# Kernel tuning notes

Hardware: AMD Instinct MI355X
Metric: run time of the kernel (lower is better)

Reference implementation:

```python
import jax, jax.numpy as jnp
import numpy as np

B, S, D_IN, D_OUT, RANK = 4, 2048, 4096, 4096, 32
BLOCK = 16
Q_MAX = 7.0  # INT4: 2**(4-1) - 1


def quantize_uniform(x, block_size=BLOCK, q_max=Q_MAX):
    """Block-wise symmetric fake-quantize (round-to-nearest, clamp)."""
    orig_shape = x.shape
    xf = x.reshape(-1, block_size)
    amax = jnp.clip(jnp.max(jnp.abs(xf), axis=-1, keepdims=True), 1e-12, None)
    scale = amax / q_max
    xq = jnp.clip(jnp.round(xf / scale), -q_max, q_max) * scale
    return xq.reshape(orig_shape)


def setup_inputs() -> dict:
    key = jax.random.key(0)
    ks = jax.random.split(key, 7)
    x = jax.random.normal(ks[0], (B, S, D_IN), jnp.float32)
    smooth_scale = jax.random.uniform(ks[1], (D_IN,), jnp.float32, 0.5, 2.0)
    w_quantized = jax.random.normal(ks[2], (D_OUT, D_IN), jnp.float32) * 0.02
    lora_a = jax.random.normal(ks[3], (RANK, D_IN), jnp.float32) * 0.02
    lora_b = jax.random.normal(ks[4], (D_OUT, RANK), jnp.float32) * 0.02
    w_sparse = jax.random.normal(ks[5], (D_OUT, D_IN), jnp.float32) * 0.02
    bias = jax.random.normal(ks[6], (D_OUT,), jnp.float32) * 0.02
    return {"x": x, "smooth_scale": smooth_scale, "w_quantized": w_quantized,
            "lora_a": lora_a, "lora_b": lora_b, "w_sparse": w_sparse, "bias": bias}


def reference(x, smooth_scale, w_quantized, lora_a, lora_b, w_sparse, bias):
    # smoothing (SmoothQuant-style per-channel scale)
    x_smoothed = x * smooth_scale                      # [B,S,Din]
    # block-wise INT4 fake-quantize of the smoothed activations
    x_q = quantize_uniform(x_smoothed)                 # [B,S,Din]
    # quantized main path
    base_out = jnp.einsum('bsi,oi->bso', x_q, w_quantized)
    # low-rank SVD error-correction path
    svd_out = jnp.einsum('bsr,or->bso',
                         jnp.einsum('bsi,ri->bsr', x_smoothed, lora_a),
                         lora_b)
    # sparse-outlier path (unsmoothed x)
    sparse_out = jnp.einsum('bsi,oi->bso', x, w_sparse)
    return base_out + svd_out + sparse_out + bias
```

## Files before the change

kernel.cpp:

```cpp
#include <hip/hip_runtime.h>
#include <stdint.h>

typedef float  f32x4  __attribute__((ext_vector_type(4)));
typedef __bf16 bf16x8 __attribute__((ext_vector_type(8)));
typedef unsigned int   u32;
typedef unsigned short u16;
typedef unsigned long long u64;
typedef u32 u32x4 __attribute__((ext_vector_type(4)));

#define M_TOT 8192
#define N_TOT 4096
#define K_DIN 4096
#define RANK  32
#define KCAT  8320
#define NTILE 130

__device__ __forceinline__ u16 f2bf(float f) {
  union { float f; u32 u; } v; v.f = f;
  u32 r = v.u + 0x7fffu + ((v.u >> 16) & 1u);
  return (u16)(r >> 16);
}

__global__ void prep_as_k(const float* __restrict__ la, const float* __restrict__ ss,
                          u16* __restrict__ asb) {
  int i = blockIdx.x * 256 + threadIdx.x;
  f32x4 v = ((const f32x4*)la)[i];
  f32x4 s = ((const f32x4*)ss)[i & 1023];
  f32x4 p = v * s;
  alignas(8) u16 o[4] = { f2bf(p[0]), f2bf(p[1]), f2bf(p[2]), f2bf(p[3]) };
  *(u64*)(asb + 4 * (size_t)i) = *(const u64*)o;
}

__global__ void cvt_w_k(const float* __restrict__ in, u16* __restrict__ Bb, int colofs) {
  int i = blockIdx.x * 256 + threadIdx.x;
  f32x4 v = ((const f32x4*)in)[i];
  int r = i >> 10, c = (i & 1023) * 4;
  alignas(8) u16 o[4] = { f2bf(v[0]), f2bf(v[1]), f2bf(v[2]), f2bf(v[3]) };
  *(u64*)(Bb + (size_t)r * KCAT + colofs + c) = *(const u64*)o;
}

__global__ void cvt_lb_k(const float* __restrict__ in, u16* __restrict__ Bb) {
  int i = blockIdx.x * 256 + threadIdx.x;
  f32x4 v = ((const f32x4*)in)[i];
  int row = i >> 3, c = (i & 7) * 4;
  alignas(8) u16 o[4] = { f2bf(v[0]), f2bf(v[1]), f2bf(v[2]), f2bf(v[3]) };
  u16* rp = Bb + (size_t)row * KCAT;
  *(u64*)(rp + 2 * K_DIN + c) = *(const u64*)o;
  u16* zp = rp + 2 * K_DIN + RANK + (i & 7) * 12;
  *(u64*)(zp + 0) = 0; *(u64*)(zp + 4) = 0; *(u64*)(zp + 8) = 0;
}

__global__ void prep_x_k(const float* __restrict__ x, const float* __restrict__ ss,
                         u16* __restrict__ Ab) {
  int m = blockIdx.x;
  int t = threadIdx.x;
  const f32x4* xp = (const f32x4*)(x + (size_t)m * K_DIN + t * 16);
  const f32x4* sp = (const f32x4*)(ss + t * 16);
  float xs[16];
  alignas(16) u16 rb[16], qb[16];
  float amax = 0.0f;
  #pragma unroll
  for (int i = 0; i < 4; ++i) {
    f32x4 a = xp[i], s = sp[i];
    #pragma unroll
    for (int j = 0; j < 4; ++j) {
      float xr = a[j];
      float v  = xr * s[j];
      xs[i*4+j] = v;
      amax = fmaxf(amax, fabsf(v));
      rb[i*4+j] = f2bf(xr);
    }
  }
  amax = fmaxf(amax, 1e-12f);
  float scale = amax / 7.0f;
  #pragma unroll
  for (int i = 0; i < 16; ++i) {
    float r = rintf(xs[i] / scale);
    r = fminf(7.0f, fmaxf(-7.0f, r));
    qb[i] = f2bf(r * scale);
  }
  u16* qo = Ab + (size_t)m * KCAT + t * 16;
  ((u32x4*)qo)[0] = ((const u32x4*)qb)[0];
  ((u32x4*)qo)[1] = ((const u32x4*)qb)[1];
  u16* ro = qo + K_DIN;
  ((u32x4*)ro)[0] = ((const u32x4*)rb)[0];
  ((u32x4*)ro)[1] = ((const u32x4*)rb)[1];
}

__global__ __launch_bounds__(256)
void lora_t_mfma_k(u16* __restrict__ Ab, const u16* __restrict__ asb) {
  const int wave = threadIdx.x >> 6;
  const int lane = threadIdx.x & 63;
  const int lr = lane & 15, lg = lane >> 4;
  const int m0 = blockIdx.x * 64 + wave * 16;
  f32x4 acc0 = {}, acc1 = {};
  for (int k0 = 0; k0 < K_DIN; k0 += 32) {
    bf16x8 a  = *(const bf16x8*)(Ab + (size_t)(m0 + lr) * KCAT + K_DIN + k0 + lg * 8);
    bf16x8 b0 = *(const bf16x8*)(asb + (size_t)lr        * K_DIN + k0 + lg * 8);
    bf16x8 b1 = *(const bf16x8*)(asb + (size_t)(16 + lr) * K_DIN + k0 + lg * 8);
    acc0 = __builtin_amdgcn_mfma_f32_16x16x32_bf16(a, b0, acc0, 0, 0, 0);
    acc1 = __builtin_amdgcn_mfma_f32_16x16x32_bf16(a, b1, acc1, 0, 0, 0);
  }
  #pragma unroll
  for (int j = 0; j < 4; ++j) {
    const int row = m0 + lg * 4 + j;
    Ab[(size_t)row * KCAT + 2 * K_DIN + lr]      = f2bf(acc0[j]);
    Ab[(size_t)row * KCAT + 2 * K_DIN + 16 + lr] = f2bf(acc1[j]);
  }
  const int zr = blockIdx.x * 64 + (threadIdx.x >> 2);
  u16* zp = Ab + (size_t)zr * KCAT + 2 * K_DIN + RANK + (threadIdx.x & 3) * 24;
  #pragma unroll
  for (int q = 0; q < 6; ++q) *(u64*)(zp + q * 4) = 0;
}

__device__ __forceinline__ void gld_lds16(const u16* g, u16* l) {
  __builtin_amdgcn_global_load_lds((const __attribute__((address_space(1))) u32*)g,
                                   (__attribute__((address_space(3))) u32*)l,
                                   16, 0, 0);
}

#define BAR()  __builtin_amdgcn_s_barrier()
#define VMW6() asm volatile("s_waitcnt vmcnt(6)" ::: "memory")
#define BUF1 32768

#define LDA(bufel, mh) do { _Pragma("unroll")                                        \
  for (int m_ = 0; m_ < 4; ++m_) {                                                   \
    Ar[m_][0] = *(const bf16x8*)(smem + (bufel) + aoff + ((mh)*4+m_)*1024 + blk0);    \
    Ar[m_][1] = *(const bf16x8*)(smem + (bufel) + aoff + ((mh)*4+m_)*1024 + blk1);    \
  } } while (0)

#define LDB(bufel, nh) do { _Pragma("unroll")                                        \
  for (int n_ = 0; n_ < 2; ++n_) {                                                   \
    Br[(nh)*2+n_][0] = *(const bf16x8*)(smem + (bufel) + boff + ((nh)*2+n_)*1024 + blk0); \
    Br[(nh)*2+n_][1] = *(const bf16x8*)(smem + (bufel) + boff + ((nh)*2+n_)*1024 + blk1); \
  } } while (0)

#define MMQ(mh, nh) do {                                                             \
  __builtin_amdgcn_s_setprio(1);                                                     \
  _Pragma("unroll")                                                                  \
  for (int m_ = 0; m_ < 4; ++m_) { _Pragma("unroll")                                 \
    for (int n_ = 0; n_ < 2; ++n_) {                                                 \
      acc[(mh)*4+m_][(nh)*2+n_] = __builtin_amdgcn_mfma_f32_16x16x32_bf16(           \
          Ar[m_][0], Br[(nh)*2+n_][0], acc[(mh)*4+m_][(nh)*2+n_], 0, 0, 0);          \
      acc[(mh)*4+m_][(nh)*2+n_] = __builtin_amdgcn_mfma_f32_16x16x32_bf16(           \
          Ar[m_][1], Br[(nh)*2+n_][1], acc[(mh)*4+m_][(nh)*2+n_], 0, 0, 0);          \
    } }                                                                              \
  __builtin_amdgcn_s_setprio(0);                                                     \
} while (0)

__global__ __launch_bounds__(512, 2)
void gemm8_k(const u16* __restrict__ Ab, const u16* __restrict__ Bb,
             const float* __restrict__ bias, float* __restrict__ out) {
  extern __shared__ u16 smem[];
  const int tid  = threadIdx.x;
  const int wave = tid >> 6;
  const int lane = tid & 63;
  const int lr = lane & 15, lg = lane >> 4;
  const int wm = wave >> 2, wn = wave & 3;

  const int wg  = blockIdx.x;
  const int swz = (wg & 7) * 64 + (wg >> 3);
  const int m0 = (swz >> 4) * 256;
  const int n0 = (swz & 15) * 256;

  const int aoff = wm * 8192 + lr * 64;
  const int boff = 16384 + wn * 4096 + lr * 64;
  const int e7   = lr & 7;
  const int blk0 = ((0 + lg) ^ e7) * 8;
  const int blk1 = ((4 + lg) ^ e7) * 8;

  const int srow = tid >> 3;
  const int scol = ((tid & 7) ^ (srow & 7)) * 8;
  const int woff = wave * 512;

  const u16* aRow = Ab + (size_t)(m0 + srow) * KCAT + scol;
  const u16* bRow = Bb + (size_t)(n0 + srow) * KCAT + scol;
  u16* dstA0 = smem + woff;
  u16* dstB0 = smem + 16384 + woff;

  bf16x8 Ar[4][2], Br[4][2];
  f32x4 acc[8][4] = {};

  auto stgA = [&](int kof, int h, int bufel) {
    u16* dst = dstA0 + bufel + h * 8192;
    gld_lds16(aRow + (size_t)(h * 128) * KCAT + kof, dst);
    gld_lds16(aRow + (size_t)(h * 128 + 64) * KCAT + kof, dst + 4096);
  };
  auto stgB = [&](int kof, int h, int bufel) {
    u16* dst = dstB0 + bufel + h * 8192;
    gld_lds16(bRow + (size_t)(h * 128) * KCAT + kof, dst);
    gld_lds16(bRow + (size_t)(h * 128 + 64) * KCAT + kof, dst + 4096);
  };

  stgA(0, 0, 0);     stgA(0, 1, 0);
  stgB(0, 0, 0);     stgB(0, 1, 0);
  stgB(64, 0, BUF1); stgB(64, 1, BUF1);
  stgA(64, 0, BUF1);
  VMW6();
  BAR();

  for (int it = 0; it < NTILE / 2; ++it) {
    const int ka = it * 128;
    int c2 = ka + 128, c3 = ka + 192;
    if (c2 > (NTILE - 1) * 64) c2 = (NTILE - 1) * 64;
    if (c3 > (NTILE - 1) * 64) c3 = (NTILE - 1) * 64;
    LDA(0, 0); LDB(0, 0);
    stgA(ka + 64, 1, BUF1);
    BAR(); MMQ(0, 0); BAR();
    LDB(0, 1);
    BAR(); MMQ(0, 1); BAR();
    LDA(0, 1);
    stgB(c2, 0, 0); stgB(c2, 1, 0);
    BAR(); MMQ(1, 1); BAR();
    stgA(c2, 0, 0);
    BAR(); MMQ(1, 0);
    VMW6();
    BAR();
    LDA(BUF1, 0); LDB(BUF1, 0);
    stgA(c2, 1, 0);
    BAR(); MMQ(0, 0); BAR();
    LDB(BUF1, 1);
    BAR(); MMQ(0, 1); BAR();
    LDA(BUF1, 1);
    stgB(c3, 0, BUF1); stgB(c3, 1, BUF1);
    BAR(); MMQ(1, 1); BAR();
    stgA(c3, 0, BUF1);
    BAR(); MMQ(1, 0);
    VMW6();
    BAR();
  }

  float bv[4];
  #pragma unroll
  for (int n = 0; n < 4; ++n) bv[n] = bias[n0 + wn * 64 + n * 16 + lr];
  #pragma unroll
  for (int m = 0; m < 8; ++m) {
    const int row = m0 + wm * 128 + m * 16 + lg * 4;
    #pragma unroll
    for (int n = 0; n < 4; ++n) {
      const int col = n0 + wn * 64 + n * 16 + lr;
      float* op = out + (size_t)row * N_TOT + col;
      op[0 * (size_t)N_TOT] = acc[m][n][0] + bv[n];
      op[1 * (size_t)N_TOT] = acc[m][n][1] + bv[n];
      op[2 * (size_t)N_TOT] = acc[m][n][2] + bv[n];
      op[3 * (size_t)N_TOT] = acc[m][n][3] + bv[n];
    }
  }
}

extern "C" void kernel_launch(void* const* d_in, const int* in_sizes, int n_in,
                              void* d_out, int out_size, void* d_ws, size_t ws_size,
                              hipStream_t stream) {
  const float* x    = (const float*)d_in[0];
  const float* ss   = (const float*)d_in[1];
  const float* wq   = (const float*)d_in[2];
  const float* la   = (const float*)d_in[3];
  const float* lb   = (const float*)d_in[4];
  const float* wsp  = (const float*)d_in[5];
  const float* bias = (const float*)d_in[6];
  float* out = (float*)d_out;

  uint8_t* w = (uint8_t*)d_ws;
  u16* Ab  = (u16*)w;  w += (size_t)M_TOT * KCAT * 2;
  u16* Bb  = (u16*)w;  w += (size_t)N_TOT * KCAT * 2;
  u16* asb = (u16*)w;

  prep_as_k<<<128, 256, 0, stream>>>(la, ss, asb);
  cvt_w_k<<<16384, 256, 0, stream>>>(wq,  Bb, 0);
  cvt_w_k<<<16384, 256, 0, stream>>>(wsp, Bb, K_DIN);
  cvt_lb_k<<<128, 256, 0, stream>>>(lb, Bb);
  prep_x_k<<<M_TOT, 256, 0, stream>>>(x, ss, Ab);
  lora_t_mfma_k<<<M_TOT / 64, 256, 0, stream>>>(Ab, asb);

  hipFuncSetAttribute((const void*)gemm8_k,
                      hipFuncAttributeMaxDynamicSharedMemorySize, 131072);
  gemm8_k<<<dim3((N_TOT / 256) * (M_TOT / 256)), 512, 131072, stream>>>(
      Ab, Bb, bias, out);
}
```

Measured before the change: 595.7 us.

## Replace 256x256 8-wave GEMM tile with 256x128 4-wave tile and K=32 stages

```diff
diff --git a/kernel.cpp b/kernel.cpp
--- a/kernel.cpp
+++ b/kernel.cpp
@@ -13,7 +13,8 @@
 #define K_DIN 4096
 #define RANK  32
 #define KCAT  8320
-#define NTILE 130
+#define NT32  260
+#define KL32  8288
 
 __device__ __forceinline__ u16 f2bf(float f) {
   union { float f; u32 u; } v; v.f = f;
@@ -120,113 +121,102 @@
 }
 
 #define BAR()  __builtin_amdgcn_s_barrier()
-#define VMW6() asm volatile("s_waitcnt vmcnt(6)" ::: "memory")
-#define BUF1 32768
+#define VMW4() asm volatile("s_waitcnt vmcnt(4)" ::: "memory")
+#define BUF1 12288
 
 #define LDA(bufel, mh) do { _Pragma("unroll")                                        \
-  for (int m_ = 0; m_ < 4; ++m_) {                                                   \
-    Ar[m_][0] = *(const bf16x8*)(smem + (bufel) + aoff + ((mh)*4+m_)*1024 + blk0);    \
-    Ar[m_][1] = *(const bf16x8*)(smem + (bufel) + aoff + ((mh)*4+m_)*1024 + blk1);    \
-  } } while (0)
+  for (int m_ = 0; m_ < 4; ++m_)                                                     \
+    Ar[m_] = *(const bf16x8*)(smem + (bufel) + aoff + (mh)*2048 + m_*512);           \
+  } while (0)
 
 #define LDB(bufel, nh) do { _Pragma("unroll")                                        \
-  for (int n_ = 0; n_ < 2; ++n_) {                                                   \
-    Br[(nh)*2+n_][0] = *(const bf16x8*)(smem + (bufel) + boff + ((nh)*2+n_)*1024 + blk0); \
-    Br[(nh)*2+n_][1] = *(const bf16x8*)(smem + (bufel) + boff + ((nh)*2+n_)*1024 + blk1); \
-  } } while (0)
+  for (int n_ = 0; n_ < 2; ++n_)                                                     \
+    Br[(nh)*2+n_] = *(const bf16x8*)(smem + (bufel) + boff + (nh)*1024 + n_*512);     \
+  } while (0)
 
 #define MMQ(mh, nh) do {                                                             \
   __builtin_amdgcn_s_setprio(1);                                                     \
   _Pragma("unroll")                                                                  \
   for (int m_ = 0; m_ < 4; ++m_) { _Pragma("unroll")                                 \
-    for (int n_ = 0; n_ < 2; ++n_) {                                                 \
+    for (int n_ = 0; n_ < 2; ++n_)                                                   \
       acc[(mh)*4+m_][(nh)*2+n_] = __builtin_amdgcn_mfma_f32_16x16x32_bf16(           \
-          Ar[m_][0], Br[(nh)*2+n_][0], acc[(mh)*4+m_][(nh)*2+n_], 0, 0, 0);          \
-      acc[(mh)*4+m_][(nh)*2+n_] = __builtin_amdgcn_mfma_f32_16x16x32_bf16(           \
-          Ar[m_][1], Br[(nh)*2+n_][1], acc[(mh)*4+m_][(nh)*2+n_], 0, 0, 0);          \
-    } }                                                                              \
+          Ar[m_], Br[(nh)*2+n_], acc[(mh)*4+m_][(nh)*2+n_], 0, 0, 0);                \
+  }                                                                                  \
   __builtin_amdgcn_s_setprio(0);                                                     \
 } while (0)
 
-__global__ __launch_bounds__(512, 2)
-void gemm8_k(const u16* __restrict__ Ab, const u16* __restrict__ Bb,
-             const float* __restrict__ bias, float* __restrict__ out) {
-  extern __shared__ u16 smem[];
+__global__ __launch_bounds__(256, 2)
+void gemm2b_k(const u16* __restrict__ Ab, const u16* __restrict__ Bb,
+              const float* __restrict__ bias, float* __restrict__ out) {
+  __shared__ u16 smem[24576];
   const int tid  = threadIdx.x;
   const int wave = tid >> 6;
   const int lane = tid & 63;
   const int lr = lane & 15, lg = lane >> 4;
-  const int wm = wave >> 2, wn = wave & 3;
+  const int wm = wave >> 1, wn = wave & 1;
 
   const int wg  = blockIdx.x;
-  const int swz = (wg & 7) * 64 + (wg >> 3);
-  const int m0 = (swz >> 4) * 256;
-  const int n0 = (swz & 15) * 256;
-
-  const int aoff = wm * 8192 + lr * 64;
-  const int boff = 16384 + wn * 4096 + lr * 64;
-  const int e7   = lr & 7;
-  const int blk0 = ((0 + lg) ^ e7) * 8;
-  const int blk1 = ((4 + lg) ^ e7) * 8;
-
-  const int srow = tid >> 3;
-  const int scol = ((tid & 7) ^ (srow & 7)) * 8;
-  const int woff = wave * 512;
+  const int swz = (wg & 7) * 128 + (wg >> 3);
+  const int m0 = (swz >> 5) * 256;
+  const int n0 = (swz & 31) * 128;
+
+  const int kx   = (lg ^ ((lr >> 2) & 3)) * 8;
+  const int aoff = (wm * 128 + lr) * 32 + kx;
+  const int boff = 8192 + (wn * 64 + lr) * 32 + kx;
+
+  const int srow = tid >> 2;
+  const int scol = ((tid & 3) ^ ((tid >> 4) & 3)) * 8;
 
   const u16* aRow = Ab + (size_t)(m0 + srow) * KCAT + scol;
   const u16* bRow = Bb + (size_t)(n0 + srow) * KCAT + scol;
-  u16* dstA0 = smem + woff;
-  u16* dstB0 = smem + 16384 + woff;
-
-  bf16x8 Ar[4][2], Br[4][2];
+  u16* dstA = smem + tid * 8;
+  u16* dstB = smem + 8192 + tid * 8;
+
+  bf16x8 Ar[4], Br[4];
   f32x4 acc[8][4] = {};
 
   auto stgA = [&](int kof, int h, int bufel) {
-    u16* dst = dstA0 + bufel + h * 8192;
-    gld_lds16(aRow + (size_t)(h * 128) * KCAT + kof, dst);
-    gld_lds16(aRow + (size_t)(h * 128 + 64) * KCAT + kof, dst + 4096);
+    gld_lds16(aRow + (size_t)(h * 64) * KCAT + kof, dstA + bufel + h * 2048);
   };
   auto stgB = [&](int kof, int h, int bufel) {
-    u16* dst = dstB0 + bufel + h * 8192;
-    gld_lds16(bRow + (size_t)(h * 128) * KCAT + kof, dst);
-    gld_lds16(bRow + (size_t)(h * 128 + 64) * KCAT + kof, dst + 4096);
+    gld_lds16(bRow + (size_t)(h * 64) * KCAT + kof, dstB + bufel + h * 2048);
   };
 
-  stgA(0, 0, 0);     stgA(0, 1, 0);
-  stgB(0, 0, 0);     stgB(0, 1, 0);
-  stgB(64, 0, BUF1); stgB(64, 1, BUF1);
-  stgA(64, 0, BUF1);
-  VMW6();
+  stgA(0, 0, 0);  stgA(0, 1, 0);  stgA(0, 2, 0);  stgA(0, 3, 0);
+  stgB(0, 0, 0);  stgB(0, 1, 0);
+  stgB(32, 0, BUF1); stgB(32, 1, BUF1);
+  stgA(32, 0, BUF1); stgA(32, 2, BUF1);
+  VMW4();
   BAR();
 
-  for (int it = 0; it < NTILE / 2; ++it) {
-    const int ka = it * 128;
-    int c2 = ka + 128, c3 = ka + 192;
-    if (c2 > (NTILE - 1) * 64) c2 = (NTILE - 1) * 64;
-    if (c3 > (NTILE - 1) * 64) c3 = (NTILE - 1) * 64;
+  for (int it = 0; it < NT32 / 2; ++it) {
+    const int ka = it * 64;
+    int c2 = ka + 64, c3 = ka + 96;
+    if (c2 > KL32) c2 = KL32;
+    if (c3 > KL32) c3 = KL32;
     LDA(0, 0); LDB(0, 0);
-    stgA(ka + 64, 1, BUF1);
+    stgA(ka + 32, 1, BUF1); stgA(ka + 32, 3, BUF1);
     BAR(); MMQ(0, 0); BAR();
     LDB(0, 1);
     BAR(); MMQ(0, 1); BAR();
     LDA(0, 1);
     stgB(c2, 0, 0); stgB(c2, 1, 0);
     BAR(); MMQ(1, 1); BAR();
-    stgA(c2, 0, 0);
+    stgA(c2, 0, 0); stgA(c2, 2, 0);
     BAR(); MMQ(1, 0);
-    VMW6();
+    VMW4();
     BAR();
     LDA(BUF1, 0); LDB(BUF1, 0);
-    stgA(c2, 1, 0);
+    stgA(c2, 1, 0); stgA(c2, 3, 0);
     BAR(); MMQ(0, 0); BAR();
     LDB(BUF1, 1);
     BAR(); MMQ(0, 1); BAR();
     LDA(BUF1, 1);
     stgB(c3, 0, BUF1); stgB(c3, 1, BUF1);
     BAR(); MMQ(1, 1); BAR();
-    stgA(c3, 0, BUF1);
+    stgA(c3, 0, BUF1); stgA(c3, 2, BUF1);
     BAR(); MMQ(1, 0);
-    VMW6();
+    VMW4();
     BAR();
   }
 
@@ -272,8 +262,6 @@
   prep_x_k<<<M_TOT, 256, 0, stream>>>(x, ss, Ab);
   lora_t_mfma_k<<<M_TOT / 64, 256, 0, stream>>>(Ab, asb);
 
-  hipFuncSetAttribute((const void*)gemm8_k,
-                      hipFuncAttributeMaxDynamicSharedMemorySize, 131072);
-  gemm8_k<<<dim3((N_TOT / 256) * (M_TOT / 256)), 512, 131072, stream>>>(
+  gemm2b_k<<<dim3((M_TOT / 256) * (N_TOT / 128)), 256, 0, stream>>>(
       Ab, Bb, bias, out);
 }
```

Result: slower. 724.6 us (+21.6%).

## Double-buffer A fragments in registers to overlap LDS reads with MFMA

Applied to the files above, without the earlier changes.

```diff
diff --git a/kernel.cpp b/kernel.cpp
--- a/kernel.cpp
+++ b/kernel.cpp
@@ -14,6 +14,7 @@
 #define RANK  32
 #define KCAT  8320
 #define NTILE 130
+#define KLAST 8256
 
 __device__ __forceinline__ u16 f2bf(float f) {
   union { float f; u32 u; } v; v.f = f;
@@ -120,13 +121,14 @@
 }
 
 #define BAR()  __builtin_amdgcn_s_barrier()
+#define SB0()  __builtin_amdgcn_sched_barrier(0)
 #define VMW6() asm volatile("s_waitcnt vmcnt(6)" ::: "memory")
 #define BUF1 32768
 
-#define LDA(bufel, mh) do { _Pragma("unroll")                                        \
+#define LDAS(AR, bufel, mh) do { _Pragma("unroll")                                   \
   for (int m_ = 0; m_ < 4; ++m_) {                                                   \
-    Ar[m_][0] = *(const bf16x8*)(smem + (bufel) + aoff + ((mh)*4+m_)*1024 + blk0);    \
-    Ar[m_][1] = *(const bf16x8*)(smem + (bufel) + aoff + ((mh)*4+m_)*1024 + blk1);    \
+    AR[m_][0] = *(const bf16x8*)(smem + (bufel) + aoff + ((mh)*4+m_)*1024 + blk0);    \
+    AR[m_][1] = *(const bf16x8*)(smem + (bufel) + aoff + ((mh)*4+m_)*1024 + blk1);    \
   } } while (0)
 
 #define LDB(bufel, nh) do { _Pragma("unroll")                                        \
@@ -135,15 +137,15 @@
     Br[(nh)*2+n_][1] = *(const bf16x8*)(smem + (bufel) + boff + ((nh)*2+n_)*1024 + blk1); \
   } } while (0)
 
-#define MMQ(mh, nh) do {                                                             \
+#define MMQ(AR, mh, nh) do {                                                         \
   __builtin_amdgcn_s_setprio(1);                                                     \
   _Pragma("unroll")                                                                  \
   for (int m_ = 0; m_ < 4; ++m_) { _Pragma("unroll")                                 \
     for (int n_ = 0; n_ < 2; ++n_) {                                                 \
       acc[(mh)*4+m_][(nh)*2+n_] = __builtin_amdgcn_mfma_f32_16x16x32_bf16(           \
-          Ar[m_][0], Br[(nh)*2+n_][0], acc[(mh)*4+m_][(nh)*2+n_], 0, 0, 0);          \
+          AR[m_][0], Br[(nh)*2+n_][0], acc[(mh)*4+m_][(nh)*2+n_], 0, 0, 0);          \
       acc[(mh)*4+m_][(nh)*2+n_] = __builtin_amdgcn_mfma_f32_16x16x32_bf16(           \
-          Ar[m_][1], Br[(nh)*2+n_][1], acc[(mh)*4+m_][(nh)*2+n_], 0, 0, 0);          \
+          AR[m_][1], Br[(nh)*2+n_][1], acc[(mh)*4+m_][(nh)*2+n_], 0, 0, 0);          \
     } }                                                                              \
   __builtin_amdgcn_s_setprio(0);                                                     \
 } while (0)
@@ -178,7 +180,7 @@
   u16* dstA0 = smem + woff;
   u16* dstB0 = smem + 16384 + woff;
 
-  bf16x8 Ar[4][2], Br[4][2];
+  bf16x8 ArA[4][2], ArB[4][2], Br[4][2];
   f32x4 acc[8][4] = {};
 
   auto stgA = [&](int kof, int h, int bufel) {
@@ -198,36 +200,42 @@
   stgA(64, 0, BUF1);
   VMW6();
   BAR();
+  SB0();
+  LDAS(ArA, 0, 0);
 
   for (int it = 0; it < NTILE / 2; ++it) {
     const int ka = it * 128;
     int c2 = ka + 128, c3 = ka + 192;
-    if (c2 > (NTILE - 1) * 64) c2 = (NTILE - 1) * 64;
-    if (c3 > (NTILE - 1) * 64) c3 = (NTILE - 1) * 64;
-    LDA(0, 0); LDB(0, 0);
+    if (c2 > KLAST) c2 = KLAST;
+    if (c3 > KLAST) c3 = KLAST;
+    LDB(0, 0);
     stgA(ka + 64, 1, BUF1);
-    BAR(); MMQ(0, 0); BAR();
+    BAR(); MMQ(ArA, 0, 0); BAR();
     LDB(0, 1);
-    BAR(); MMQ(0, 1); BAR();
-    LDA(0, 1);
+    LDAS(ArB, 0, 1);
+    BAR(); MMQ(ArA, 0, 1); BAR();
     stgB(c2, 0, 0); stgB(c2, 1, 0);
-    BAR(); MMQ(1, 1); BAR();
+    BAR(); MMQ(ArB, 1, 1); BAR();
     stgA(c2, 0, 0);
-    BAR(); MMQ(1, 0);
     VMW6();
     BAR();
-    LDA(BUF1, 0); LDB(BUF1, 0);
+    SB0();
+    LDAS(ArA, BUF1, 0);
+    MMQ(ArB, 1, 0); BAR();
+    LDB(BUF1, 0);
+    LDAS(ArB, BUF1, 1);
     stgA(c2, 1, 0);
-    BAR(); MMQ(0, 0); BAR();
+    BAR(); MMQ(ArA, 0, 0); BAR();
     LDB(BUF1, 1);
-    BAR(); MMQ(0, 1); BAR();
-    LDA(BUF1, 1);
+    BAR(); MMQ(ArA, 0, 1); BAR();
     stgB(c3, 0, BUF1); stgB(c3, 1, BUF1);
-    BAR(); MMQ(1, 1); BAR();
+    BAR(); MMQ(ArB, 1, 1); BAR();
     stgA(c3, 0, BUF1);
-    BAR(); MMQ(1, 0);
     VMW6();
     BAR();
+    SB0();
+    LDAS(ArA, 0, 0);
+    MMQ(ArB, 1, 0); BAR();
   }
 
   float bv[4];
```

Measured after the change: 608.9 us. +2.2%, slower.

## Merge weight prep launches and coarsen GEMM MFMA phases to halve barriers

Applied to the files above, without the earlier changes.

```diff
diff --git a/kernel.cpp b/kernel.cpp
--- a/kernel.cpp
+++ b/kernel.cpp
@@ -14,6 +14,7 @@
 #define RANK  32
 #define KCAT  8320
 #define NTILE 130
+#define KLAST 8256
 
 __device__ __forceinline__ u16 f2bf(float f) {
   union { float f; u32 u; } v; v.f = f;
@@ -21,33 +22,37 @@
   return (u16)(r >> 16);
 }
 
-__global__ void prep_as_k(const float* __restrict__ la, const float* __restrict__ ss,
-                          u16* __restrict__ asb) {
-  int i = blockIdx.x * 256 + threadIdx.x;
-  f32x4 v = ((const f32x4*)la)[i];
-  f32x4 s = ((const f32x4*)ss)[i & 1023];
-  f32x4 p = v * s;
-  alignas(8) u16 o[4] = { f2bf(p[0]), f2bf(p[1]), f2bf(p[2]), f2bf(p[3]) };
-  *(u64*)(asb + 4 * (size_t)i) = *(const u64*)o;
-}
-
-__global__ void cvt_w_k(const float* __restrict__ in, u16* __restrict__ Bb, int colofs) {
-  int i = blockIdx.x * 256 + threadIdx.x;
-  f32x4 v = ((const f32x4*)in)[i];
-  int r = i >> 10, c = (i & 1023) * 4;
-  alignas(8) u16 o[4] = { f2bf(v[0]), f2bf(v[1]), f2bf(v[2]), f2bf(v[3]) };
-  *(u64*)(Bb + (size_t)r * KCAT + colofs + c) = *(const u64*)o;
-}
-
-__global__ void cvt_lb_k(const float* __restrict__ in, u16* __restrict__ Bb) {
-  int i = blockIdx.x * 256 + threadIdx.x;
-  f32x4 v = ((const f32x4*)in)[i];
-  int row = i >> 3, c = (i & 7) * 4;
-  alignas(8) u16 o[4] = { f2bf(v[0]), f2bf(v[1]), f2bf(v[2]), f2bf(v[3]) };
-  u16* rp = Bb + (size_t)row * KCAT;
-  *(u64*)(rp + 2 * K_DIN + c) = *(const u64*)o;
-  u16* zp = rp + 2 * K_DIN + RANK + (i & 7) * 12;
-  *(u64*)(zp + 0) = 0; *(u64*)(zp + 4) = 0; *(u64*)(zp + 8) = 0;
+__global__ void prep_b_k(const float* __restrict__ wq, const float* __restrict__ wsp,
+                         const float* __restrict__ lb, const float* __restrict__ la,
+                         const float* __restrict__ ss,
+                         u16* __restrict__ Bb, u16* __restrict__ asb) {
+  const int b = blockIdx.x;
+  const int tid = threadIdx.x;
+  if (b < 32768) {
+    const float* src = (b < 16384) ? wq : wsp;
+    const int colofs = (b < 16384) ? 0 : K_DIN;
+    const int i = (b & 16383) * 256 + tid;
+    f32x4 v = ((const f32x4*)src)[i];
+    int r = i >> 10, c = (i & 1023) * 4;
+    alignas(8) u16 o[4] = { f2bf(v[0]), f2bf(v[1]), f2bf(v[2]), f2bf(v[3]) };
+    *(u64*)(Bb + (size_t)r * KCAT + colofs + c) = *(const u64*)o;
+  } else if (b < 32896) {
+    const int i = (b - 32768) * 256 + tid;
+    f32x4 v = ((const f32x4*)lb)[i];
+    int row = i >> 3, c = (i & 7) * 4;
+    alignas(8) u16 o[4] = { f2bf(v[0]), f2bf(v[1]), f2bf(v[2]), f2bf(v[3]) };
+    u16* rp = Bb + (size_t)row * KCAT;
+    *(u64*)(rp + 2 * K_DIN + c) = *(const u64*)o;
+    u16* zp = rp + 2 * K_DIN + RANK + (i & 7) * 12;
+    *(u64*)(zp + 0) = 0; *(u64*)(zp + 4) = 0; *(u64*)(zp + 8) = 0;
+  } else {
+    const int i = (b - 32896) * 256 + tid;
+    f32x4 v = ((const f32x4*)la)[i];
+    f32x4 s = ((const f32x4*)ss)[i & 1023];
+    f32x4 p = v * s;
+    alignas(8) u16 o[4] = { f2bf(p[0]), f2bf(p[1]), f2bf(p[2]), f2bf(p[3]) };
+    *(u64*)(asb + 4 * (size_t)i) = *(const u64*)o;
+  }
 }
 
 __global__ void prep_x_k(const float* __restrict__ x, const float* __restrict__ ss,
@@ -135,15 +140,15 @@
     Br[(nh)*2+n_][1] = *(const bf16x8*)(smem + (bufel) + boff + ((nh)*2+n_)*1024 + blk1); \
   } } while (0)
 
-#define MMQ(mh, nh) do {                                                             \
+#define MMQ2(mh) do {                                                                \
   __builtin_amdgcn_s_setprio(1);                                                     \
   _Pragma("unroll")                                                                  \
   for (int m_ = 0; m_ < 4; ++m_) { _Pragma("unroll")                                 \
-    for (int n_ = 0; n_ < 2; ++n_) {                                                 \
-      acc[(mh)*4+m_][(nh)*2+n_] = __builtin_amdgcn_mfma_f32_16x16x32_bf16(           \
-          Ar[m_][0], Br[(nh)*2+n_][0], acc[(mh)*4+m_][(nh)*2+n_], 0, 0, 0);          \
-      acc[(mh)*4+m_][(nh)*2+n_] = __builtin_amdgcn_mfma_f32_16x16x32_bf16(           \
-          Ar[m_][1], Br[(nh)*2+n_][1], acc[(mh)*4+m_][(nh)*2+n_], 0, 0, 0);          \
+    for (int n_ = 0; n_ < 4; ++n_) {                                                 \
+      acc[(mh)*4+m_][n_] = __builtin_amdgcn_mfma_f32_16x16x32_bf16(                  \
+          Ar[m_][0], Br[n_][0], acc[(mh)*4+m_][n_], 0, 0, 0);                        \
+      acc[(mh)*4+m_][n_] = __builtin_amdgcn_mfma_f32_16x16x32_bf16(                  \
+          Ar[m_][1], Br[n_][1], acc[(mh)*4+m_][n_], 0, 0, 0);                        \
     } }                                                                              \
   __builtin_amdgcn_s_setprio(0);                                                     \
 } while (0)
@@ -202,30 +207,22 @@
   for (int it = 0; it < NTILE / 2; ++it) {
     const int ka = it * 128;
     int c2 = ka + 128, c3 = ka + 192;
-    if (c2 > (NTILE - 1) * 64) c2 = (NTILE - 1) * 64;
-    if (c3 > (NTILE - 1) * 64) c3 = (NTILE - 1) * 64;
-    LDA(0, 0); LDB(0, 0);
+    if (c2 > KLAST) c2 = KLAST;
+    if (c3 > KLAST) c3 = KLAST;
+    LDA(0, 0); LDB(0, 0); LDB(0, 1);
     stgA(ka + 64, 1, BUF1);
-    BAR(); MMQ(0, 0); BAR();
-    LDB(0, 1);
-    BAR(); MMQ(0, 1); BAR();
+    BAR(); MMQ2(0); BAR();
     LDA(0, 1);
-    stgB(c2, 0, 0); stgB(c2, 1, 0);
-    BAR(); MMQ(1, 1); BAR();
-    stgA(c2, 0, 0);
-    BAR(); MMQ(1, 0);
+    stgB(c2, 0, 0); stgB(c2, 1, 0); stgA(c2, 0, 0);
+    BAR(); MMQ2(1);
     VMW6();
     BAR();
-    LDA(BUF1, 0); LDB(BUF1, 0);
+    LDA(BUF1, 0); LDB(BUF1, 0); LDB(BUF1, 1);
     stgA(c2, 1, 0);
-    BAR(); MMQ(0, 0); BAR();
-    LDB(BUF1, 1);
-    BAR(); MMQ(0, 1); BAR();
+    BAR(); MMQ2(0); BAR();
     LDA(BUF1, 1);
-    stgB(c3, 0, BUF1); stgB(c3, 1, BUF1);
-    BAR(); MMQ(1, 1); BAR();
-    stgA(c3, 0, BUF1);
-    BAR(); MMQ(1, 0);
+    stgB(c3, 0, BUF1); stgB(c3, 1, BUF1); stgA(c3, 0, BUF1);
+    BAR(); MMQ2(1);
     VMW6();
     BAR();
   }
@@ -265,10 +262,7 @@
   u16* Bb  = (u16*)w;  w += (size_t)N_TOT * KCAT * 2;
   u16* asb = (u16*)w;
 
-  prep_as_k<<<128, 256, 0, stream>>>(la, ss, asb);
-  cvt_w_k<<<16384, 256, 0, stream>>>(wq,  Bb, 0);
-  cvt_w_k<<<16384, 256, 0, stream>>>(wsp, Bb, K_DIN);
-  cvt_lb_k<<<128, 256, 0, stream>>>(lb, Bb);
+  prep_b_k<<<33024, 256, 0, stream>>>(wq, wsp, lb, la, ss, Bb, asb);
   prep_x_k<<<M_TOT, 256, 0, stream>>>(x, ss, Ab);
   lora_t_mfma_k<<<M_TOT / 64, 256, 0, stream>>>(Ab, asb);
 
```

Result: slower. 608.5 us (+2.2%).
